# Optimization experiments

Hardware: AMD Instinct MI355X
Metric: run time of the kernel (lower is better)

Reference implementation:

```python
import jax, jax.numpy as jnp
import numpy as np
from jax import lax

NEG = -1e30  # acts as log(0) without producing nan gradients


def setup_inputs() -> dict:
    key = jax.random.key(0)
    k1, k2 = jax.random.split(key)
    B, T, C, L = 128, 2000, 62, 256
    inputs = jax.random.normal(k1, (B, T, C), dtype=jnp.float32)
    targets = jax.random.randint(k2, (B, L), 0, C, dtype=jnp.int32)
    return {"inputs": inputs, "targets": targets}


def _transducer_loss(inputs, targets):
    # ngram=0 path: log-softmax normalize emissions (as in Transducer.forward)
    lp = jax.nn.log_softmax(inputs, axis=2)            # [B, T, C]
    lp_t = jnp.transpose(lp, (1, 0, 2))                # [T, B, C]
    B, L = targets.shape

    # Alignment lattice (tokens graph with self-loops, blank=False,
    # allow_repeats=True, identity lexicon): each target label must be
    # emitted on >= 1 consecutive frames, monotonically.
    # alpha[b, u] = log-sum of all alignments of frames 0..t ending at label u.
    em0 = jnp.take_along_axis(lp_t[0], targets, axis=1)         # [B, L]
    u = jnp.arange(L)
    alpha0 = jnp.where(u[None, :] == 0, em0, NEG)                # [B, L]

    def step(alpha, lp_bt):
        em = jnp.take_along_axis(lp_bt, targets, axis=1)         # [B, L]
        prev = jnp.pad(alpha[:, :-1], ((0, 0), (1, 0)), constant_values=NEG)
        alpha = jnp.logaddexp(alpha, prev) + em                  # stay or advance
        return alpha, None

    alpha, _ = lax.scan(step, alpha0, lp_t[1:])
    per_seq_loss = -alpha[:, -1]                                 # [B]
    # TransducerLossFunction returns torch.mean over the batch
    return jnp.mean(per_seq_loss)


def reference(inputs, targets):
    return _transducer_loss(inputs, targets)
```

## Files before the change

kernel.cpp:

```cpp
#include <hip/hip_runtime.h>
#include <hip/hip_bf16.h>

#define NEGF (-1e30f)
#define INVLN2 1.4426950408889634f
#define LN2F 0.6931471805599453f

#if __has_builtin(__builtin_amdgcn_exp2f)
#define FEXP2(x) __builtin_amdgcn_exp2f(x)
#else
#define FEXP2(x) exp2f(x)
#endif
#if __has_builtin(__builtin_amdgcn_logf)
#define FLOG2(x) __builtin_amdgcn_logf(x)
#else
#define FLOG2(x) __log2f(x)
#endif

__device__ __forceinline__ float shr1_neg(float v) {
  return __int_as_float(__builtin_amdgcn_update_dpp(
      __float_as_int(NEGF), __float_as_int(v), 0x138, 0xf, 0xf, false));
}
#define ROR16(v, n) __int_as_float(__builtin_amdgcn_update_dpp(          \
    __float_as_int(v), __float_as_int(v), 0x120 + (n), 0xf, 0xf, false))
#define BCAST(v, c) __int_as_float(__builtin_amdgcn_update_dpp(          \
    __float_as_int(v), __float_as_int(v), (c), 0xf, 0xf, false))

__device__ __forceinline__ float l2ae(float p, float q) {
  float m = fmaxf(p, q);
  float z = -fabsf(p - q);
  return m + FLOG2(1.0f + FEXP2(z));
}

__global__ __launch_bounds__(256) void lse_kernel(const float* __restrict__ x,
                                                  float* __restrict__ lse) {
  int gid = blockIdx.x * 256 + threadIdx.x;
  int grp = gid >> 4;
  int k = gid & 15;
  const char* rb = (const char*)x + (size_t)grp * 248;
  float2 va = *(const float2*)(rb + 8 * k);
  float2 vb = *(const float2*)(rb + 128 + 8 * (k < 14 ? k : 14));
  if (k == 15) { vb.x = NEGF; vb.y = NEGF; }
  float m = fmaxf(fmaxf(va.x, va.y), fmaxf(vb.x, vb.y));
  m = fmaxf(m, ROR16(m, 1)); m = fmaxf(m, ROR16(m, 2));
  m = fmaxf(m, ROR16(m, 4)); m = fmaxf(m, ROR16(m, 8));
  float mi = -m * INVLN2;
  float s = FEXP2(fmaf(va.x, INVLN2, mi)) + FEXP2(fmaf(va.y, INVLN2, mi))
          + FEXP2(fmaf(vb.x, INVLN2, mi)) + FEXP2(fmaf(vb.y, INVLN2, mi));
  s += ROR16(s, 1); s += ROR16(s, 2); s += ROR16(s, 4); s += ROR16(s, 8);
  if (k == 0) lse[grp] = fmaf(FLOG2(s), LN2F, m);
}

__global__ __launch_bounds__(256) void sum_kernel(const float* __restrict__ lse,
                                                  float* __restrict__ sums,
                                                  float* __restrict__ out) {
  const int T = 2000;
  int b = blockIdx.x;
  int tid = threadIdx.x;
  if (b == 0 && tid == 0) out[0] = 0.0f;
  float s = 0.f;
  for (int t = tid; t < T; t += 256) s += lse[(size_t)b * T + t];
  #pragma unroll
  for (int off = 32; off >= 1; off >>= 1) s += __shfl_xor(s, off, 64);
  __shared__ float wsum[4];
  if ((tid & 63) == 0) wsum[tid >> 6] = s;
  __syncthreads();
  if (tid == 0) sums[b] = wsum[0] + wsum[1] + wsum[2] + wsum[3];
}

template <int SGN>
__device__ __forceinline__ float4 do_scan(const char* p0, const char* p1,
                                          const char* p2, const char* p3,
                                          int lane) {
  const int RB = 248;
  float e00 = *(const float*)p0;
  float a0 = (lane == 0) ? e00 * INVLN2 : NEGF;
  float a1 = NEGF, a2 = NEGF, a3 = NEGF;

  #define BANK(B) float B##0, B##1, B##2, B##3;
  BANK(h0) BANK(h1) BANK(h2) BANK(h3) BANK(h4) BANK(h5) BANK(h6) BANK(h7)
  BANK(h8) BANK(h9) BANK(hA) BANK(hB) BANK(hC) BANK(hD) BANK(hE) BANK(hF)
  #undef BANK

  #define GATHER(B, OFS) {                        \
    B##0 = *(const float*)(p0 + (OFS));           \
    B##1 = *(const float*)(p1 + (OFS));           \
    B##2 = *(const float*)(p2 + (OFS));           \
    B##3 = *(const float*)(p3 + (OFS));           \
  }
  #define CONS(B) {                                                 \
    float pm = shr1_neg(a3);                                        \
    float m0 = fmaxf(a0, pm); float z0 = -fabsf(a0 - pm);           \
    float m1 = fmaxf(a1, a0); float z1 = -fabsf(a1 - a0);           \
    float m2 = fmaxf(a2, a1); float z2 = -fabsf(a2 - a1);           \
    float m3 = fmaxf(a3, a2); float z3 = -fabsf(a3 - a2);           \
    a0 = fmaf(B##0, INVLN2, m0 + FLOG2(1.0f + FEXP2(z0)));          \
    a1 = fmaf(B##1, INVLN2, m1 + FLOG2(1.0f + FEXP2(z1)));          \
    a2 = fmaf(B##2, INVLN2, m2 + FLOG2(1.0f + FEXP2(z2)));          \
    a3 = fmaf(B##3, INVLN2, m3 + FLOG2(1.0f + FEXP2(z3)));          \
  }
  #define GRP(A, B, C, D) {                                         \
    p0 += SGN * 4 * RB; p1 += SGN * 4 * RB;                         \
    p2 += SGN * 4 * RB; p3 += SGN * 4 * RB;                         \
    CONS(A) GATHER(A, SGN * 13 * RB)                                \
    CONS(B) GATHER(B, SGN * 14 * RB)                                \
    CONS(C) GATHER(C, SGN * 15 * RB)                                \
    CONS(D) GATHER(D, SGN * 16 * RB)                                \
  }

  GATHER(h0, SGN *  1 * RB) GATHER(h1, SGN *  2 * RB)
  GATHER(h2, SGN *  3 * RB) GATHER(h3, SGN *  4 * RB)
  GATHER(h4, SGN *  5 * RB) GATHER(h5, SGN *  6 * RB)
  GATHER(h6, SGN *  7 * RB) GATHER(h7, SGN *  8 * RB)
  GATHER(h8, SGN *  9 * RB) GATHER(h9, SGN * 10 * RB)
  GATHER(hA, SGN * 11 * RB) GATHER(hB, SGN * 12 * RB)
  GATHER(hC, SGN * 13 * RB) GATHER(hD, SGN * 14 * RB)
  GATHER(hE, SGN * 15 * RB) GATHER(hF, SGN * 16 * RB)

  #pragma unroll 1
  for (int j = 0; j < 62; ++j) {
    GRP(h0, h1, h2, h3)
    GRP(h4, h5, h6, h7)
    GRP(h8, h9, hA, hB)
    GRP(hC, hD, hE, hF)
  }
  CONS(h0) CONS(h1) CONS(h2) CONS(h3) CONS(h4) CONS(h5) CONS(h6)
  #undef GATHER
  #undef CONS
  #undef GRP
  return make_float4(a0, a1, a2, a3);
}

__global__ __launch_bounds__(64) void scan_kernel(const float* __restrict__ x,
                                                  const int* __restrict__ tg,
                                                  float* __restrict__ wsA,
                                                  float* __restrict__ wsB) {
  const int T = 2000, C = 62, L = 256;
  const int RB = C * 4;
  int b = blockIdx.x >> 1;
  int dir = blockIdx.x & 1;
  int lane = threadIdx.x;
  const char* xb = (const char*)(x + (size_t)b * T * C);

  if (dir == 0) {
    int4 t4 = ((const int4*)(tg + (size_t)b * L))[lane];
    float4 r = do_scan<1>(xb + (t4.x << 2), xb + (t4.y << 2),
                          xb + (t4.z << 2), xb + (t4.w << 2), lane);
    ((float4*)(wsA + (size_t)b * 256))[lane] = r;
  } else {
    int4 t4 = ((const int4*)(tg + (size_t)b * L))[63 - lane];
    const char* base = xb + 1999 * RB;
    float4 r = do_scan<-1>(base + (t4.w << 2), base + (t4.z << 2),
                           base + (t4.y << 2), base + (t4.x << 2), lane);
    ((float4*)(wsB + (size_t)b * 272))[63 - lane] = make_float4(r.w, r.z, r.y, r.x);
    if (lane == 0) wsB[(size_t)b * 272 + 256] = NEGF;
  }
}

__global__ __launch_bounds__(64) void combine_kernel(const float* __restrict__ wsA,
                                                     const float* __restrict__ wsB,
                                                     const float* __restrict__ sums,
                                                     float* __restrict__ out) {
  int b = blockIdx.x;
  int l = threadIdx.x;
  float4 av = ((const float4*)(wsA + (size_t)b * 256))[l];
  float4 bv = ((const float4*)(wsB + (size_t)b * 272))[l];
  float bx = (wsB + (size_t)b * 272)[4 * l + 4];
  float c0 = av.x + l2ae(bv.x, bv.y);
  float c1 = av.y + l2ae(bv.y, bv.z);
  float c2 = av.z + l2ae(bv.z, bv.w);
  float c3 = av.w + l2ae(bv.w, bx);
  float m = fmaxf(fmaxf(c0, c1), fmaxf(c2, c3));
  m = fmaxf(m, ROR16(m, 1)); m = fmaxf(m, ROR16(m, 2));
  m = fmaxf(m, ROR16(m, 4)); m = fmaxf(m, ROR16(m, 8));
  m = fmaxf(m, BCAST(m, 0x142)); m = fmaxf(m, BCAST(m, 0x143));
  float M = __int_as_float(__builtin_amdgcn_readlane(__float_as_int(m), 63));
  float s = FEXP2(c0 - M) + FEXP2(c1 - M) + FEXP2(c2 - M) + FEXP2(c3 - M);
  s += ROR16(s, 1); s += ROR16(s, 2); s += ROR16(s, 4); s += ROR16(s, 8);
  s += BCAST(s, 0x142); s += BCAST(s, 0x143);
  if (l == 63) {
    float A_ln = (M + FLOG2(s)) * LN2F;
    atomicAdd(out, (sums[b] - A_ln) * (1.0f / 128.0f));
  }
}

extern "C" void kernel_launch(void* const* d_in, const int* in_sizes, int n_in,
                              void* d_out, int out_size, void* d_ws, size_t ws_size,
                              hipStream_t stream) {
  const float* x  = (const float*)d_in[0];
  const int*   tg = (const int*)d_in[1];
  float* out  = (float*)d_out;
  float* lse  = (float*)d_ws;
  float* wsA  = lse;
  float* wsB  = lse + 40960;
  float* sums = lse + 256000;

  lse_kernel<<<16000, 256, 0, stream>>>(x, lse);
  sum_kernel<<<128, 256, 0, stream>>>(lse, sums, out);
  scan_kernel<<<256, 64, 0, stream>>>(x, tg, wsA, wsB);
  combine_kernel<<<128, 64, 0, stream>>>(wsA, wsB, sums, out);
}
```

Before: 191.4 us.

## Fuse LSE with per-sequence sums and combine into scan; gather emissions via bpermute

Folds the per-row log-sum-exp into block-level partial sums, which removes the separate sum kernel. The forward and backward scans now run as two waves of one block, and the combine step happens in-kernel through shared memory, which drops the combine launch and the global workspace round trip. The scan also stops doing four scattered per-lane gathers per timestep. Each lane instead loads one coalesced class column of the row and picks the target emissions with ds_bpermute, using a deeper 32-row register prefetch ring. This trades cross-lane permute traffic and more register pressure for fewer scattered memory accesses and fewer launches.

```diff
diff --git a/kernel.cpp b/kernel.cpp
--- a/kernel.cpp
+++ b/kernel.cpp
@@ -16,6 +16,9 @@
 #define FLOG2(x) __log2f(x)
 #endif
 
+__device__ __forceinline__ float bp(int addr, float v) {
+  return __int_as_float(__builtin_amdgcn_ds_bpermute(addr, __float_as_int(v)));
+}
 __device__ __forceinline__ float shr1_neg(float v) {
   return __int_as_float(__builtin_amdgcn_update_dpp(
       __float_as_int(NEGF), __float_as_int(v), 0x138, 0xf, 0xf, false));
@@ -31,12 +34,17 @@
   return m + FLOG2(1.0f + FEXP2(z));
 }
 
-__global__ __launch_bounds__(256) void lse_kernel(const float* __restrict__ x,
-                                                  float* __restrict__ lse) {
-  int gid = blockIdx.x * 256 + threadIdx.x;
-  int grp = gid >> 4;
-  int k = gid & 15;
-  const char* rb = (const char*)x + (size_t)grp * 248;
+__global__ __launch_bounds__(256) void lse_sum_kernel(const float* __restrict__ x,
+                                                      float* __restrict__ partial,
+                                                      float* __restrict__ out) {
+  int blk = blockIdx.x;
+  int b = blk / 125, i = blk - 125 * b;
+  int tid = threadIdx.x;
+  int k = tid & 15;
+  int row = b * 2000 + i * 16 + (tid >> 4);
+  if (blk == 0 && tid == 0) out[0] = 0.0f;
+
+  const char* rb = (const char*)x + (size_t)row * 248;
   float2 va = *(const float2*)(rb + 8 * k);
   float2 vb = *(const float2*)(rb + 128 + 8 * (k < 14 ? k : 14));
   if (k == 15) { vb.x = NEGF; vb.y = NEGF; }
@@ -47,124 +55,106 @@
   float s = FEXP2(fmaf(va.x, INVLN2, mi)) + FEXP2(fmaf(va.y, INVLN2, mi))
           + FEXP2(fmaf(vb.x, INVLN2, mi)) + FEXP2(fmaf(vb.y, INVLN2, mi));
   s += ROR16(s, 1); s += ROR16(s, 2); s += ROR16(s, 4); s += ROR16(s, 8);
-  if (k == 0) lse[grp] = fmaf(FLOG2(s), LN2F, m);
-}
-
-__global__ __launch_bounds__(256) void sum_kernel(const float* __restrict__ lse,
-                                                  float* __restrict__ sums,
-                                                  float* __restrict__ out) {
-  const int T = 2000;
-  int b = blockIdx.x;
-  int tid = threadIdx.x;
-  if (b == 0 && tid == 0) out[0] = 0.0f;
-  float s = 0.f;
-  for (int t = tid; t < T; t += 256) s += lse[(size_t)b * T + t];
+  float v = fmaf(FLOG2(s), LN2F, m) * (1.0f / 16.0f);
   #pragma unroll
-  for (int off = 32; off >= 1; off >>= 1) s += __shfl_xor(s, off, 64);
-  __shared__ float wsum[4];
-  if ((tid & 63) == 0) wsum[tid >> 6] = s;
+  for (int off = 32; off >= 1; off >>= 1) v += __shfl_xor(v, off, 64);
+  __shared__ float ws4[4];
+  if ((tid & 63) == 0) ws4[tid >> 6] = v;
   __syncthreads();
-  if (tid == 0) sums[b] = wsum[0] + wsum[1] + wsum[2] + wsum[3];
+  if (tid == 0) partial[b * 128 + i] = ws4[0] + ws4[1] + ws4[2] + ws4[3];
 }
 
 template <int SGN>
-__device__ __forceinline__ float4 do_scan(const char* p0, const char* p1,
-                                          const char* p2, const char* p3,
+__device__ __forceinline__ float4 do_scan(const float* __restrict__ xb,
+                                          int ta0, int ta1, int ta2, int ta3,
                                           int lane) {
-  const int RB = 248;
-  float e00 = *(const float*)p0;
-  float a0 = (lane == 0) ? e00 * INVLN2 : NEGF;
+  const int RW = 62;
+  int cc = lane < 62 ? lane : 0;
+  const float* base = xb + (SGN > 0 ? 0 : 1999 * RW) + cc;
+
+  float g0row = base[0] * INVLN2;
+  float a0 = (lane == 0) ? bp(ta0, g0row) : NEGF;
   float a1 = NEGF, a2 = NEGF, a3 = NEGF;
 
-  #define BANK(B) float B##0, B##1, B##2, B##3;
-  BANK(h0) BANK(h1) BANK(h2) BANK(h3) BANK(h4) BANK(h5) BANK(h6) BANK(h7)
-  BANK(h8) BANK(h9) BANK(hA) BANK(hB) BANK(hC) BANK(hD) BANK(hE) BANK(hF)
-  #undef BANK
+  float r[32];
+  float bk[4][4];
 
-  #define GATHER(B, OFS) {                        \
-    B##0 = *(const float*)(p0 + (OFS));           \
-    B##1 = *(const float*)(p1 + (OFS));           \
-    B##2 = *(const float*)(p2 + (OFS));           \
-    B##3 = *(const float*)(p3 + (OFS));           \
-  }
-  #define CONS(B) {                                                 \
-    float pm = shr1_neg(a3);                                        \
-    float m0 = fmaxf(a0, pm); float z0 = -fabsf(a0 - pm);           \
-    float m1 = fmaxf(a1, a0); float z1 = -fabsf(a1 - a0);           \
-    float m2 = fmaxf(a2, a1); float z2 = -fabsf(a2 - a1);           \
-    float m3 = fmaxf(a3, a2); float z3 = -fabsf(a3 - a2);           \
-    a0 = fmaf(B##0, INVLN2, m0 + FLOG2(1.0f + FEXP2(z0)));          \
-    a1 = fmaf(B##1, INVLN2, m1 + FLOG2(1.0f + FEXP2(z1)));          \
-    a2 = fmaf(B##2, INVLN2, m2 + FLOG2(1.0f + FEXP2(z2)));          \
-    a3 = fmaf(B##3, INVLN2, m3 + FLOG2(1.0f + FEXP2(z3)));          \
-  }
-  #define GRP(A, B, C, D) {                                         \
-    p0 += SGN * 4 * RB; p1 += SGN * 4 * RB;                         \
-    p2 += SGN * 4 * RB; p3 += SGN * 4 * RB;                         \
-    CONS(A) GATHER(A, SGN * 13 * RB)                                \
-    CONS(B) GATHER(B, SGN * 14 * RB)                                \
-    CONS(C) GATHER(C, SGN * 15 * RB)                                \
-    CONS(D) GATHER(D, SGN * 16 * RB)                                \
+  #pragma unroll
+  for (int i = 0; i < 32; ++i) r[i] = base[SGN * (i + 1) * RW];
+  r[0] *= INVLN2; r[1] *= INVLN2; r[2] *= INVLN2; r[3] *= INVLN2;
+  #define BPERM(S, RS) {                              \
+    bk[S][0] = bp(ta0, RS); bk[S][1] = bp(ta1, RS);   \
+    bk[S][2] = bp(ta2, RS); bk[S][3] = bp(ta3, RS); }
+  BPERM(0, r[0]) BPERM(1, r[1]) BPERM(2, r[2])
+
+  const float* lp = base + SGN * 33 * RW;
+
+  #define CONS(S) {                                            \
+    float pm = shr1_neg(a3);                                   \
+    float m0 = fmaxf(a0, pm), z0 = a0 - pm;                    \
+    float m1 = fmaxf(a1, a0), z1 = a1 - a0;                    \
+    float m2 = fmaxf(a2, a1), z2 = a2 - a1;                    \
+    float m3 = fmaxf(a3, a2), z3 = a3 - a2;                    \
+    a0 = m0 + FLOG2(1.0f + FEXP2(-fabsf(z0))) + bk[S][0];      \
+    a1 = m1 + FLOG2(1.0f + FEXP2(-fabsf(z1))) + bk[S][1];      \
+    a2 = m2 + FLOG2(1.0f + FEXP2(-fabsf(z2))) + bk[S][2];      \
+    a3 = m3 + FLOG2(1.0f + FEXP2(-fabsf(z3))) + bk[S][3];      \
   }
 
-  GATHER(h0, SGN *  1 * RB) GATHER(h1, SGN *  2 * RB)
-  GATHER(h2, SGN *  3 * RB) GATHER(h3, SGN *  4 * RB)
-  GATHER(h4, SGN *  5 * RB) GATHER(h5, SGN *  6 * RB)
-  GATHER(h6, SGN *  7 * RB) GATHER(h7, SGN *  8 * RB)
-  GATHER(h8, SGN *  9 * RB) GATHER(h9, SGN * 10 * RB)
-  GATHER(hA, SGN * 11 * RB) GATHER(hB, SGN * 12 * RB)
-  GATHER(hC, SGN * 13 * RB) GATHER(hD, SGN * 14 * RB)
-  GATHER(hE, SGN * 15 * RB) GATHER(hF, SGN * 16 * RB)
+  #pragma unroll 1
+  for (int g = 0; g < 31; ++g) {
+    #pragma unroll
+    for (int j = 0; j < 32; ++j) {
+      BPERM((j + 3) & 3, r[(j + 3) & 31])
+      r[(j + 4) & 31] *= INVLN2;
+      r[j] = *lp; lp += SGN * RW;
+      CONS(j & 3)
+    }
+  }
+  CONS(0) BPERM(3, r[3]) r[4] *= INVLN2;
+  CONS(1) BPERM(0, r[4]) r[5] *= INVLN2;
+  CONS(2) BPERM(1, r[5]) r[6] *= INVLN2;
+  CONS(3) BPERM(2, r[6])
+  CONS(0)
+  CONS(1)
+  CONS(2)
+  #undef BPERM
+  #undef CONS
 
-  #pragma unroll 1
-  for (int j = 0; j < 62; ++j) {
-    GRP(h0, h1, h2, h3)
-    GRP(h4, h5, h6, h7)
-    GRP(h8, h9, hA, hB)
-    GRP(hC, hD, hE, hF)
-  }
-  CONS(h0) CONS(h1) CONS(h2) CONS(h3) CONS(h4) CONS(h5) CONS(h6)
-  #undef GATHER
-  #undef CONS
-  #undef GRP
   return make_float4(a0, a1, a2, a3);
 }
 
-__global__ __launch_bounds__(64) void scan_kernel(const float* __restrict__ x,
-                                                  const int* __restrict__ tg,
-                                                  float* __restrict__ wsA,
-                                                  float* __restrict__ wsB) {
+__global__ __launch_bounds__(128) void scan_kernel(const float* __restrict__ x,
+                                                   const int* __restrict__ tg,
+                                                   const float* __restrict__ partial,
+                                                   float* __restrict__ out) {
   const int T = 2000, C = 62, L = 256;
-  const int RB = C * 4;
-  int b = blockIdx.x >> 1;
-  int dir = blockIdx.x & 1;
-  int lane = threadIdx.x;
-  const char* xb = (const char*)(x + (size_t)b * T * C);
+  int b = blockIdx.x;
+  int tid = threadIdx.x;
+  int wid = tid >> 6, lane = tid & 63;
+  const float* xb = x + (size_t)b * T * C;
 
-  if (dir == 0) {
+  __shared__ float sbeta[257];
+  float4 av;
+
+  if (wid == 0) {
     int4 t4 = ((const int4*)(tg + (size_t)b * L))[lane];
-    float4 r = do_scan<1>(xb + (t4.x << 2), xb + (t4.y << 2),
-                          xb + (t4.z << 2), xb + (t4.w << 2), lane);
-    ((float4*)(wsA + (size_t)b * 256))[lane] = r;
+    av = do_scan<1>(xb, t4.x << 2, t4.y << 2, t4.z << 2, t4.w << 2, lane);
   } else {
     int4 t4 = ((const int4*)(tg + (size_t)b * L))[63 - lane];
-    const char* base = xb + 1999 * RB;
-    float4 r = do_scan<-1>(base + (t4.w << 2), base + (t4.z << 2),
-                           base + (t4.y << 2), base + (t4.x << 2), lane);
-    ((float4*)(wsB + (size_t)b * 272))[63 - lane] = make_float4(r.w, r.z, r.y, r.x);
-    if (lane == 0) wsB[(size_t)b * 272 + 256] = NEGF;
+    float4 r = do_scan<-1>(xb, t4.w << 2, t4.z << 2, t4.y << 2, t4.x << 2, lane);
+    ((float4*)sbeta)[63 - lane] = make_float4(r.w, r.z, r.y, r.x);
+    if (lane == 0) sbeta[256] = NEGF;
   }
-}
+  __syncthreads();
+  if (wid != 0) return;
 
-__global__ __launch_bounds__(64) void combine_kernel(const float* __restrict__ wsA,
-                                                     const float* __restrict__ wsB,
-                                                     const float* __restrict__ sums,
-                                                     float* __restrict__ out) {
-  int b = blockIdx.x;
-  int l = threadIdx.x;
-  float4 av = ((const float4*)(wsA + (size_t)b * 256))[l];
-  float4 bv = ((const float4*)(wsB + (size_t)b * 272))[l];
-  float bx = (wsB + (size_t)b * 272)[4 * l + 4];
+  float p = partial[b * 128 + lane] + partial[b * 128 + 64 + lane];
+  #pragma unroll
+  for (int o = 32; o >= 1; o >>= 1) p += __shfl_xor(p, o, 64);
+
+  float4 bv = ((const float4*)sbeta)[lane];
+  float bx = sbeta[4 * lane + 4];
   float c0 = av.x + l2ae(bv.x, bv.y);
   float c1 = av.y + l2ae(bv.y, bv.z);
   float c2 = av.z + l2ae(bv.z, bv.w);
@@ -177,9 +167,9 @@
   float s = FEXP2(c0 - M) + FEXP2(c1 - M) + FEXP2(c2 - M) + FEXP2(c3 - M);
   s += ROR16(s, 1); s += ROR16(s, 2); s += ROR16(s, 4); s += ROR16(s, 8);
   s += BCAST(s, 0x142); s += BCAST(s, 0x143);
-  if (l == 63) {
+  if (lane == 63) {
     float A_ln = (M + FLOG2(s)) * LN2F;
-    atomicAdd(out, (sums[b] - A_ln) * (1.0f / 128.0f));
+    atomicAdd(out, (p - A_ln) * (1.0f / 128.0f));
   }
 }
 
@@ -188,14 +178,9 @@
                               hipStream_t stream) {
   const float* x  = (const float*)d_in[0];
   const int*   tg = (const int*)d_in[1];
-  float* out  = (float*)d_out;
-  float* lse  = (float*)d_ws;
-  float* wsA  = lse;
-  float* wsB  = lse + 40960;
-  float* sums = lse + 256000;
+  float* out     = (float*)d_out;
+  float* partial = (float*)d_ws;
 
-  lse_kernel<<<16000, 256, 0, stream>>>(x, lse);
-  sum_kernel<<<128, 256, 0, stream>>>(lse, sums, out);
-  scan_kernel<<<256, 64, 0, stream>>>(x, tg, wsA, wsB);
-  combine_kernel<<<128, 64, 0, stream>>>(wsA, wsB, sums, out);
+  lse_sum_kernel<<<16000, 256, 0, stream>>>(x, partial, out);
+  scan_kernel<<<128, 128, 0, stream>>>(x, tg, partial, out);
 }
```

Result: faster. 186.9 us (-2.4%).
